# Kernel tuning notes

Measured on AMD Instinct MI355X. Metric: run time of the kernel, lower is better.

The kernel has to match this reference:

```python
import jax, jax.numpy as jnp
import numpy as np

B, N, FIN, FOUT = 8, 4096, 64, 64
NEG_SLOPE = 0.01  # torch LeakyReLU default


def setup_inputs() -> dict:
    key = jax.random.key(0)
    k1, k2, k3, k4, k5 = jax.random.split(key, 5)
    inp = jax.random.normal(k1, (B, N, FIN), dtype=jnp.float32)
    adj = jax.random.randint(k2, (N, N), 0, 2, dtype=jnp.int32)
    W_w = jax.random.normal(k3, (FOUT, FIN), dtype=jnp.float32) * (1.0 / np.sqrt(FIN))
    W_b = jax.random.normal(k4, (FOUT,), dtype=jnp.float32) * 0.01
    a = jax.random.normal(k5, (2 * FOUT, N), dtype=jnp.float32) * (1.414 / np.sqrt(2 * FOUT + N))
    return {"inp": inp, "adj": adj, "W_w": W_w, "W_b": W_b, "a": a}


def reference(inp, adj, W_w, W_b, a):
    # h = W(inp); h[:, 0, :] = 0
    h = jnp.einsum('bnf,of->bno', inp, W_w) + W_b          # [B, N, F]
    h = h.at[:, 0, :].set(0.0)

    # Original loop: for i in 1..N-1:
    #   ac = a[:, i]  (shape [2F, 1])
    #   index = where(adj[1:, i] > 0)  -> 0-based, used to index h directly (bug preserved)
    #   s_i = h[:, i, :] @ ac[:F] + sum_j h[:, index, :] @ ac[F:]   (scalar per batch)
    #   attention[:, i, :] = s_i broadcast over all columns
    # Empty-index case equals the general case since an empty neighbor sum is 0.
    mask = (adj[1:, :] > 0).astype(h.dtype)                # [N-1, N]
    neigh = jnp.einsum('ji,bjf->bif', mask, h[:, :N - 1, :])  # [B, N, F]
    s = (jnp.einsum('bif,fi->bi', h, a[:FOUT]) +
         jnp.einsum('bif,fi->bi', neigh, a[FOUT:]))        # [B, N]
    s = s.at[:, 0].set(0.0)                                # attention row 0 stays zero

    # h_prime = attention @ h, with attention[b,i,j] = s[b,i] for all j
    hsum = h.sum(axis=1)                                   # [B, F]
    h_prime = s[:, :, None] * hsum[:, None, :]             # [B, N, F]
    return jnp.where(h_prime >= 0, h_prime, NEG_SLOPE * h_prime)
```

## Files before the change

kernel.cpp:

```cpp
#include <hip/hip_runtime.h>
#include <hip/hip_bf16.h>

#define NN 4096

typedef unsigned short u16;
typedef __attribute__((ext_vector_type(8))) short short8;
typedef __attribute__((ext_vector_type(4))) float f32x4;
typedef __attribute__((ext_vector_type(4))) unsigned short u16x4;
typedef __attribute__((ext_vector_type(8))) unsigned short u16x8;
typedef __attribute__((ext_vector_type(4))) int i32x4;

typedef const void __attribute__((address_space(1)))* gas_t;
typedef void __attribute__((address_space(3)))* las_t;

__device__ __forceinline__ u16 f2bf(float x) {
  unsigned u = __float_as_uint(x);
  return (u16)((u + 0x7FFFu + ((u >> 16) & 1)) >> 16);
}

__global__ __launch_bounds__(256) void k_maskT(const int* __restrict__ adj, u16* __restrict__ maskT) {
  __shared__ __align__(16) u16 tile[128 * 132];
  const int i0 = blockIdx.x * 128, j0 = blockIdx.y * 128;
  const int t = threadIdx.x;
  const int jr = t >> 5, ic = (t & 31) * 4;
#pragma unroll
  for (int pass = 0; pass < 16; ++pass) {
    const int jl = pass * 8 + jr;
    const int j = j0 + jl;
    u16 v0 = 0, v1 = 0, v2 = 0, v3 = 0;
    if (j < NN - 1) {
      i32x4 av = *reinterpret_cast<const i32x4*>(&adj[(size_t)(j + 1) * NN + i0 + ic]);
      v0 = av.x > 0 ? 0x3F80 : 0;
      v1 = av.y > 0 ? 0x3F80 : 0;
      v2 = av.z > 0 ? 0x3F80 : 0;
      v3 = av.w > 0 ? 0x3F80 : 0;
    }
    tile[(ic + 0) * 132 + jl] = v0;
    tile[(ic + 1) * 132 + jl] = v1;
    tile[(ic + 2) * 132 + jl] = v2;
    tile[(ic + 3) * 132 + jl] = v3;
  }
  __syncthreads();
  const int ir = t >> 5, jc = (t & 31) * 4;
#pragma unroll
  for (int pass = 0; pass < 16; ++pass) {
    const int il = pass * 8 + ir;
    u16x4 o = *reinterpret_cast<const u16x4*>(&tile[il * 132 + jc]);
    *reinterpret_cast<u16x4*>(&maskT[(size_t)(i0 + il) * NN + j0 + jc]) = o;
  }
}

__global__ __launch_bounds__(256) void k_h(const float* __restrict__ inp, const float* __restrict__ Ww,
                                           const float* __restrict__ Wb, float* __restrict__ h,
                                           u16* __restrict__ h2t, float* __restrict__ hsum) {
  __shared__ __align__(16) u16 lA[128 * 64];
  __shared__ __align__(16) u16 lW[64 * 64];
  const int t = threadIdx.x, lane = t & 63, w = t >> 6;
  const int bid = blockIdx.x;
  const int b = bid >> 5;
  const size_t row0 = (size_t)bid * 128;
  {
    const int o = t >> 2, k0 = (t & 3) * 16;
    const float* src = &Ww[o * 64 + k0];
    u16 tmp[16];
#pragma unroll
    for (int e = 0; e < 16; ++e) tmp[e] = f2bf(src[e]);
    const int swz = (o & 7) * 8;
#pragma unroll
    for (int v = 0; v < 2; ++v)
      *reinterpret_cast<u16x8*>(&lW[o * 64 + ((k0 + v * 8) ^ swz)]) = *reinterpret_cast<u16x8*>(&tmp[v * 8]);
  }
  {
    const int r = t >> 1, k0 = (t & 1) * 32;
    const float* src = &inp[(row0 + r) * 64 + k0];
    u16 tmp[32];
#pragma unroll
    for (int e = 0; e < 32; ++e) tmp[e] = f2bf(src[e]);
    const int swz = (r & 7) * 8;
#pragma unroll
    for (int v = 0; v < 4; ++v)
      *reinterpret_cast<u16x8*>(&lA[r * 64 + ((k0 + v * 8) ^ swz)]) = *reinterpret_cast<u16x8*>(&tmp[v * 8]);
  }
  __syncthreads();
  f32x4 acc[2][4] = {};
#pragma unroll
  for (int ks = 0; ks < 2; ++ks) {
    const int kk = ks * 32 + (lane >> 4) * 8;
    short8 af[2], bf[4];
#pragma unroll
    for (int m = 0; m < 2; ++m) {
      const int row = w * 32 + m * 16 + (lane & 15);
      af[m] = *reinterpret_cast<const short8*>(&lA[row * 64 + (kk ^ ((row & 7) * 8))]);
    }
#pragma unroll
    for (int n = 0; n < 4; ++n) {
      const int o = n * 16 + (lane & 15);
      bf[n] = *reinterpret_cast<const short8*>(&lW[o * 64 + (kk ^ ((o & 7) * 8))]);
    }
#pragma unroll
    for (int m = 0; m < 2; ++m)
#pragma unroll
      for (int n = 0; n < 4; ++n)
        acc[m][n] = __builtin_amdgcn_mfma_f32_16x16x32_bf16(af[m], bf[n], acc[m][n], 0, 0, 0);
  }
  const int f0 = lane & 15;
  const int rsub = (lane >> 4) * 4;
  float wb[4];
#pragma unroll
  for (int n = 0; n < 4; ++n) wb[n] = Wb[n * 16 + f0];
  const int nloc_base = (bid & 31) * 128;
  float ps[4] = {0.f, 0.f, 0.f, 0.f};
#pragma unroll
  for (int m = 0; m < 2; ++m) {
    const int rl = w * 32 + m * 16 + rsub;
#pragma unroll
    for (int n = 0; n < 4; ++n) {
      u16 hb[4];
#pragma unroll
      for (int r = 0; r < 4; ++r) {
        float v = acc[m][n][r] + wb[n];
        if (nloc_base + rl + r == 0) v = 0.f;
        h[(row0 + rl + r) * 64 + n * 16 + f0] = v;
        hb[r] = f2bf(v);
        ps[n] += v;
      }
      *reinterpret_cast<u16x4*>(&h2t[(size_t)(b * 64 + n * 16 + f0) * NN + nloc_base + rl]) =
          *reinterpret_cast<u16x4*>(&hb[0]);
    }
  }
#pragma unroll
  for (int n = 0; n < 4; ++n) {
    float v = ps[n];
    v += __shfl_xor(v, 16);
    v += __shfl_xor(v, 32);
    if (lane < 16) atomicAdd(&hsum[b * 64 + n * 16 + f0], v);
  }
}

__global__ __launch_bounds__(256, 4) void k_gemm(const u16* __restrict__ A, const u16* __restrict__ Bm,
                                                 const float* __restrict__ a, float* __restrict__ s) {
  __shared__ __align__(16) u16 lA[128 * 64];
  __shared__ __align__(16) u16 lB[128 * 64];
  const int c0 = blockIdx.x * 128, i0 = blockIdx.y * 128, z = blockIdx.z;
  const int t = threadIdx.x, lane = t & 63, w = t >> 6;
  const int wr = w >> 1, wc = w & 1;

  const int srow = lane >> 3;
  const int sk = ((lane & 7) ^ srow) * 8;
  const size_t kbase = (size_t)z * 512;
  const u16* gA = A + (size_t)(i0 + w * 32 + srow) * NN + kbase + sk;
  const u16* gB = Bm + (size_t)(c0 + w * 32 + srow) * NN + kbase + sk;

  f32x4 acc[4][4] = {};
  for (int kt = 0; kt < 512; kt += 64) {
#pragma unroll
    for (int c = 0; c < 4; ++c) {
      __builtin_amdgcn_global_load_lds((gas_t)(gA + (size_t)(8 * c) * NN + kt),
                                       (las_t)((char*)lA + (w * 32 + 8 * c) * 128 + lane * 16), 16, 0, 0);
      __builtin_amdgcn_global_load_lds((gas_t)(gB + (size_t)(8 * c) * NN + kt),
                                       (las_t)((char*)lB + (w * 32 + 8 * c) * 128 + lane * 16), 16, 0, 0);
    }
    __syncthreads();
#pragma unroll
    for (int ks = 0; ks < 2; ++ks) {
      const int kb = ks * 4 + (lane >> 4);
      short8 af[4], bf[4];
#pragma unroll
      for (int m = 0; m < 4; ++m) {
        const int row = wr * 64 + m * 16 + (lane & 15);
        af[m] = *reinterpret_cast<const short8*>(&lA[row * 64 + ((kb ^ (row & 7)) * 8)]);
      }
#pragma unroll
      for (int n = 0; n < 4; ++n) {
        const int row = wc * 64 + n * 16 + (lane & 15);
        bf[n] = *reinterpret_cast<const short8*>(&lB[row * 64 + ((kb ^ (row & 7)) * 8)]);
      }
#pragma unroll
      for (int m = 0; m < 4; ++m)
#pragma unroll
        for (int n = 0; n < 4; ++n)
          acc[m][n] = __builtin_amdgcn_mfma_f32_16x16x32_bf16(af[m], bf[n], acc[m][n], 0, 0, 0);
    }
    __syncthreads();
  }
  const int b = blockIdx.x * 2 + wc;
  const int f0 = lane & 15, rsub = (lane >> 4) * 4;
  float pp[4][4];
#pragma unroll
  for (int m = 0; m < 4; ++m) {
    const int irow = i0 + wr * 64 + m * 16 + rsub;
#pragma unroll
    for (int r = 0; r < 4; ++r) pp[m][r] = 0.f;
#pragma unroll
    for (int n = 0; n < 4; ++n) {
      f32x4 a2v = *reinterpret_cast<const f32x4*>(&a[(size_t)(64 + n * 16 + f0) * NN + irow]);
#pragma unroll
      for (int r = 0; r < 4; ++r) pp[m][r] += acc[m][n][r] * a2v[r];
    }
  }
#pragma unroll
  for (int m = 0; m < 4; ++m)
#pragma unroll
    for (int r = 0; r < 4; ++r) {
      float v = pp[m][r];
      v += __shfl_xor(v, 1);
      v += __shfl_xor(v, 2);
      v += __shfl_xor(v, 4);
      v += __shfl_xor(v, 8);
      pp[m][r] = v;
    }
  if (f0 == 0) {
    const int irow = i0 + wr * 64 + rsub;
#pragma unroll
    for (int m = 0; m < 4; ++m)
#pragma unroll
      for (int r = 0; r < 4; ++r)
        atomicAdd(&s[(size_t)b * NN + irow + m * 16 + r], pp[m][r]);
  }
}

__global__ __launch_bounds__(256) void k_final(const float* __restrict__ h, const float* __restrict__ sg,
                                               const float* __restrict__ a, const float* __restrict__ hsum,
                                               float* __restrict__ out) {
  __shared__ float a1[64][65];
  __shared__ float hs[64], sv[64];
  const int b = blockIdx.x >> 6;
  const int i0 = (blockIdx.x & 63) * 64;
  const int t = threadIdx.x;
  {
    const int lr = t >> 6, li = t & 63;
#pragma unroll
    for (int rr = 0; rr < 64; rr += 4)
      a1[rr + lr][li] = a[(size_t)(rr + lr) * NN + i0 + li];
    if (t < 64) hs[t] = hsum[b * 64 + t];
  }
  __syncthreads();
  const int il = t >> 2, q = t & 3;
  const int i = i0 + il;
  const float* hrow = &h[((size_t)b * NN + i) * 64 + q * 16];
  float p = 0.f;
#pragma unroll
  for (int k = 0; k < 16; ++k) p += hrow[k] * a1[q * 16 + k][il];
  p += __shfl_down(p, 2, 4);
  p += __shfl_down(p, 1, 4);
  if (q == 0) sv[il] = (i == 0) ? 0.f : (p + sg[(size_t)b * NN + i]);
  __syncthreads();
  const int lf = t & 63, lr2 = t >> 6;
#pragma unroll
  for (int rr = 0; rr < 64; rr += 4) {
    int ii = rr + lr2;
    float val = sv[ii] * hs[lf];
    out[((size_t)b * NN + i0 + ii) * 64 + lf] = (val >= 0.f) ? val : 0.01f * val;
  }
}

extern "C" void kernel_launch(void* const* d_in, const int* in_sizes, int n_in,
                              void* d_out, int out_size, void* d_ws, size_t ws_size,
                              hipStream_t stream) {
  const float* inp = (const float*)d_in[0];
  const int* adj = (const int*)d_in[1];
  const float* Ww = (const float*)d_in[2];
  const float* Wb = (const float*)d_in[3];
  const float* a = (const float*)d_in[4];
  float* out = (float*)d_out;
  char* ws = (char*)d_ws;

  float* s = (float*)ws;
  float* hsum = (float*)(ws + 131072);
  u16* maskT = (u16*)(ws + 262144);
  u16* h2t = (u16*)(ws + 262144 + 33554432);
  float* h = (float*)(ws + 262144 + 33554432 + 4194304);

  hipMemsetAsync(ws, 0, 133120, stream);
  hipLaunchKernelGGL(k_maskT, dim3(32, 32), dim3(256), 0, stream, adj, maskT);
  hipLaunchKernelGGL(k_h, dim3(256), dim3(256), 0, stream, inp, Ww, Wb, h, h2t, hsum);
  hipLaunchKernelGGL(k_gemm, dim3(4, 32, 8), dim3(256), 0, stream, maskT, h2t, a, s);
  hipLaunchKernelGGL(k_final, dim3(512), dim3(256), 0, stream, h, s, a, hsum, out);
}
```

Before: 162.6 us.

## Double-buffer GEMM LDS tiles, halve split-K count, and remap blocks for XCD locality

The mask×h GEMM now double-buffers its LDS tiles, so global-to-LDS loads for the next K step are issued while MFMAs run on the current one. Split-K drops from 8 slices of 512 to 4 slices of 1024, halving the grid to 512 blocks. It switches to a 1D grid with a swizzled block-to-tile mapping that groups related tiles per XCD for L2 reuse. LDS per block doubles and the occupancy hint drops from 4 to 2 blocks per CU, trading latency hiding for overlap. Fewer split-K slices also means fewer atomic partial-sum contributions to s.

```diff
diff --git a/kernel.cpp b/kernel.cpp
--- a/kernel.cpp
+++ b/kernel.cpp
@@ -137,53 +137,70 @@
   }
 }
 
-__global__ __launch_bounds__(256, 4) void k_gemm(const u16* __restrict__ A, const u16* __restrict__ Bm,
+__global__ __launch_bounds__(256, 2) void k_gemm(const u16* __restrict__ A, const u16* __restrict__ Bm,
                                                  const float* __restrict__ a, float* __restrict__ s) {
-  __shared__ __align__(16) u16 lA[128 * 64];
-  __shared__ __align__(16) u16 lB[128 * 64];
-  const int c0 = blockIdx.x * 128, i0 = blockIdx.y * 128, z = blockIdx.z;
+  __shared__ __align__(16) u16 lA0[128 * 64], lA1[128 * 64];
+  __shared__ __align__(16) u16 lB0[128 * 64], lB1[128 * 64];
+  const int sid = blockIdx.x;
+  const int wgid = (sid & 7) * 64 + (sid >> 3);
+  const int c0 = (wgid & 3) * 128;
+  const int i0 = ((wgid >> 2) & 31) * 128;
+  const int z = wgid >> 7;
   const int t = threadIdx.x, lane = t & 63, w = t >> 6;
   const int wr = w >> 1, wc = w & 1;
 
   const int srow = lane >> 3;
   const int sk = ((lane & 7) ^ srow) * 8;
-  const size_t kbase = (size_t)z * 512;
+  const size_t kbase = (size_t)z * 1024;
   const u16* gA = A + (size_t)(i0 + w * 32 + srow) * NN + kbase + sk;
   const u16* gB = Bm + (size_t)(c0 + w * 32 + srow) * NN + kbase + sk;
 
+#define STAGE_K(dstA, dstB, kt)                                                              \
+  do {                                                                                       \
+    _Pragma("unroll") for (int c = 0; c < 4; ++c) {                                          \
+      __builtin_amdgcn_global_load_lds((gas_t)(gA + (size_t)(8 * c) * NN + (kt)),            \
+                                       (las_t)((dstA) + (w * 32 + 8 * c) * 128 + lane * 16), \
+                                       16, 0, 0);                                            \
+      __builtin_amdgcn_global_load_lds((gas_t)(gB + (size_t)(8 * c) * NN + (kt)),            \
+                                       (las_t)((dstB) + (w * 32 + 8 * c) * 128 + lane * 16), \
+                                       16, 0, 0);                                            \
+    }                                                                                        \
+  } while (0)
+
   f32x4 acc[4][4] = {};
-  for (int kt = 0; kt < 512; kt += 64) {
-#pragma unroll
-    for (int c = 0; c < 4; ++c) {
-      __builtin_amdgcn_global_load_lds((gas_t)(gA + (size_t)(8 * c) * NN + kt),
-                                       (las_t)((char*)lA + (w * 32 + 8 * c) * 128 + lane * 16), 16, 0, 0);
-      __builtin_amdgcn_global_load_lds((gas_t)(gB + (size_t)(8 * c) * NN + kt),
-                                       (las_t)((char*)lB + (w * 32 + 8 * c) * 128 + lane * 16), 16, 0, 0);
-    }
-    __syncthreads();
+  STAGE_K((char*)lA0, (char*)lB0, 0);
+  __syncthreads();
+#pragma unroll 1
+  for (int it = 0; it < 16; ++it) {
+    char* nA = (it & 1) ? (char*)lA0 : (char*)lA1;
+    char* nB = (it & 1) ? (char*)lB0 : (char*)lB1;
+    if (it < 15) STAGE_K(nA, nB, (it + 1) * 64);
+    const u16* cA = (it & 1) ? lA1 : lA0;
+    const u16* cB = (it & 1) ? lB1 : lB0;
 #pragma unroll
     for (int ks = 0; ks < 2; ++ks) {
       const int kb = ks * 4 + (lane >> 4);
-      short8 af[4], bf[4];
+      short8 af[4], bfr[4];
 #pragma unroll
       for (int m = 0; m < 4; ++m) {
         const int row = wr * 64 + m * 16 + (lane & 15);
-        af[m] = *reinterpret_cast<const short8*>(&lA[row * 64 + ((kb ^ (row & 7)) * 8)]);
+        af[m] = *reinterpret_cast<const short8*>(&cA[row * 64 + ((kb ^ (row & 7)) * 8)]);
       }
 #pragma unroll
       for (int n = 0; n < 4; ++n) {
         const int row = wc * 64 + n * 16 + (lane & 15);
-        bf[n] = *reinterpret_cast<const short8*>(&lB[row * 64 + ((kb ^ (row & 7)) * 8)]);
+        bfr[n] = *reinterpret_cast<const short8*>(&cB[row * 64 + ((kb ^ (row & 7)) * 8)]);
       }
 #pragma unroll
       for (int m = 0; m < 4; ++m)
 #pragma unroll
         for (int n = 0; n < 4; ++n)
-          acc[m][n] = __builtin_amdgcn_mfma_f32_16x16x32_bf16(af[m], bf[n], acc[m][n], 0, 0, 0);
+          acc[m][n] = __builtin_amdgcn_mfma_f32_16x16x32_bf16(af[m], bfr[n], acc[m][n], 0, 0, 0);
     }
     __syncthreads();
   }
-  const int b = blockIdx.x * 2 + wc;
+#undef STAGE_K
+  const int b = (c0 >> 7) * 2 + wc;
   const int f0 = lane & 15, rsub = (lane >> 4) * 4;
   float pp[4][4];
 #pragma unroll
@@ -274,6 +291,6 @@
   hipMemsetAsync(ws, 0, 133120, stream);
   hipLaunchKernelGGL(k_maskT, dim3(32, 32), dim3(256), 0, stream, adj, maskT);
   hipLaunchKernelGGL(k_h, dim3(256), dim3(256), 0, stream, inp, Ww, Wb, h, h2t, hsum);
-  hipLaunchKernelGGL(k_gemm, dim3(4, 32, 8), dim3(256), 0, stream, maskT, h2t, a, s);
+  hipLaunchKernelGGL(k_gemm, dim3(512), dim3(256), 0, stream, maskT, h2t, a, s);
   hipLaunchKernelGGL(k_final, dim3(512), dim3(256), 0, stream, h, s, a, hsum, out);
 }
```

After: 152.4 us. -6.3%, faster.
